# Kernel optimization log

Measured on AMD Instinct MI355X. Metric: run time of the kernel, lower is better.

Reference implementation:

```python
import jax, jax.numpy as jnp
import numpy as np

N_NODES = 50000
N_RAND_EDGES = 800000  # plus N_NODES self-loop edges appended in setup
IN_FEATS, N_HIDDEN, N_CLASSES = 128, 64, 64


def setup_inputs() -> dict:
    key = jax.random.key(0)
    kf, ks, kd, k1, k2, k3 = jax.random.split(key, 6)
    features = jax.random.normal(kf, (N_NODES, IN_FEATS), dtype=jnp.float32)
    src = jax.random.randint(ks, (N_RAND_EDGES,), 0, N_NODES, dtype=jnp.int32)
    dst = jax.random.randint(kd, (N_RAND_EDGES,), 0, N_NODES, dtype=jnp.int32)
    # dgl.add_self_loop: append (i, i) for every node
    loop = jnp.arange(N_NODES, dtype=jnp.int32)
    src = jnp.concatenate([src, loop])
    dst = jnp.concatenate([dst, loop])

    def glorot(k, fan_in, fan_out):
        lim = jnp.sqrt(6.0 / (fan_in + fan_out)).astype(jnp.float32)
        return jax.random.uniform(k, (fan_in, fan_out), jnp.float32, -lim, lim)

    return {
        "features": features, "src": src, "dst": dst,
        "W1": glorot(k1, IN_FEATS, N_HIDDEN), "b1": jnp.zeros((N_HIDDEN,), jnp.float32),
        "W2": glorot(k2, N_HIDDEN, N_HIDDEN), "b2": jnp.zeros((N_HIDDEN,), jnp.float32),
        "W3": glorot(k3, N_HIDDEN, N_CLASSES), "b3": jnp.zeros((N_CLASSES,), jnp.float32),
    }


def _graph_conv(x, W, b, src, dst, norm_src_e, norm_dst_n, n_nodes):
    """DGL GraphConv, norm='both': D_dst^{-1/2} A D_src^{-1/2} X W + b, then relu."""
    if W.shape[0] > W.shape[1]:  # mult by W first when it shrinks the feature dim
        x = x @ W
        m = x[src] * norm_src_e[:, None]                      # [E, out]
        h = jax.ops.segment_sum(m, dst, num_segments=n_nodes)  # [N, out]
        h = h * norm_dst_n[:, None]
    else:
        m = x[src] * norm_src_e[:, None]                      # [E, in]
        h = jax.ops.segment_sum(m, dst, num_segments=n_nodes)  # [N, in]
        h = (h * norm_dst_n[:, None]) @ W
    return jax.nn.relu(h + b)


def reference(features, src, dst, W1, b1, W2, b2, W3, b3):
    n = features.shape[0]
    ones = jnp.ones(src.shape[0], dtype=features.dtype)
    out_deg = jax.ops.segment_sum(ones, src, num_segments=n)
    in_deg = jax.ops.segment_sum(ones, dst, num_segments=n)
    norm_out = jnp.where(out_deg > 0, jax.lax.rsqrt(jnp.maximum(out_deg, 1.0)), 0.0)
    norm_in = jnp.where(in_deg > 0, jax.lax.rsqrt(jnp.maximum(in_deg, 1.0)), 0.0)
    norm_src_e = norm_out[src]  # per-edge source normalization

    h1 = _graph_conv(features, W1, b1, src, dst, norm_src_e, norm_in, n)
    h2 = _graph_conv(h1, W2, b2, src, dst, norm_src_e, norm_in, n)
    h3 = _graph_conv(h2, W3, b3, src, dst, norm_src_e, norm_in, n)
    # JumpingKnowledge mode='max': elementwise max over stacked layer outputs
    return jnp.max(jnp.stack([h1, h2, h3], axis=0), axis=0)
```

## Files before the change

### kernel.cpp

```cpp
#include <hip/hip_runtime.h>

typedef _Float16 h16;
typedef __attribute__((ext_vector_type(4))) _Float16 half4;

#define RANGES 8
#define PPR    32
#define HTHREADS 1024
#define BINS   6400
#define HALF   (BINS / 2)
#define HWORDS (BINS)

__global__ __launch_bounds__(HTHREADS) void hist_kernel(const int* __restrict__ src,
                                                        const int* __restrict__ dst,
                                                        int* __restrict__ partial, int E) {
  __shared__ int h[HWORDS];
  const int r = blockIdx.x >> 5;
  const int c = blockIdx.x & 31;
  for (int i = threadIdx.x; i < HWORDS; i += HTHREADS) h[i] = 0;
  __syncthreads();
  const int lo = r * BINS;
  const int chunk = (E + PPR - 1) / PPR;
  const int e0 = c * chunk;
  const int e1 = min(E, e0 + chunk);
  for (int e = e0 + threadIdx.x; e < e1; e += HTHREADS) {
    int s = src[e] - lo;
    if ((unsigned)s < (unsigned)BINS) atomicAdd(&h[s >> 1], 1 << ((s & 1) * 16));
    int d = dst[e] - lo;
    if ((unsigned)d < (unsigned)BINS) atomicAdd(&h[HALF + (d >> 1)], 1 << ((d & 1) * 16));
  }
  __syncthreads();
  int* op = partial + (size_t)blockIdx.x * HWORDS;
  for (int i = threadIdx.x; i < HWORDS; i += HTHREADS) op[i] = h[i];
}

__global__ __launch_bounds__(256) void reduce_norm_scan1(
    int* __restrict__ partial, float* __restrict__ nout, float* __restrict__ nin,
    int* __restrict__ rowptr, int* __restrict__ bsums, int N) {
  __shared__ int s[256];
  const int j = blockIdx.x * 256 + threadIdx.x;
  const int r = j / HALF;
  const int w = j % HALF;
  int* base = partial + (size_t)(r * PPR) * HWORDS;
  int sumO = 0, runI = 0;
#pragma unroll 8
  for (int p = 0; p < PPR; ++p) {
    sumO += base[(size_t)p * HWORDS + w];
    int vI = base[(size_t)p * HWORDS + HALF + w];
    base[(size_t)p * HWORDS + HALF + w] = runI;
    runI += vI;
  }
  const int od0 = sumO & 0xFFFF, od1 = (sumO >> 16) & 0xFFFF;
  const int id0 = runI & 0xFFFF, id1 = (runI >> 16) & 0xFFFF;
  const int n0 = 2 * j, n1 = 2 * j + 1;
  if (n0 < N) {
    nout[n0] = od0 > 0 ? rsqrtf((float)od0) : 0.f;
    nin[n0]  = id0 > 0 ? rsqrtf((float)id0) : 0.f;
  }
  if (n1 < N) {
    nout[n1] = od1 > 0 ? rsqrtf((float)od1) : 0.f;
    nin[n1]  = id1 > 0 ? rsqrtf((float)id1) : 0.f;
  }
  const int local = id0 + id1;
  int v = local;
  s[threadIdx.x] = v;
  __syncthreads();
#pragma unroll
  for (int off = 1; off < 256; off <<= 1) {
    int tv = 0;
    if (threadIdx.x >= off) tv = s[threadIdx.x - off];
    __syncthreads();
    if (threadIdx.x >= off) s[threadIdx.x] += tv;
    __syncthreads();
  }
  const int excl = s[threadIdx.x] - v;
  if (n0 < N) rowptr[n0] = excl;
  if (n1 < N) rowptr[n1] = excl + id0;
  if (threadIdx.x == 255) bsums[blockIdx.x] = s[255];
}

__global__ void scan_top(int* __restrict__ bsums, int nb) {
  __shared__ int s[256];
  __shared__ int run_s;
  if (threadIdx.x == 0) run_s = 0;
  __syncthreads();
  for (int base = 0; base < nb; base += 256) {
    int i = base + threadIdx.x;
    int v = (i < nb) ? bsums[i] : 0;
    s[threadIdx.x] = v;
    __syncthreads();
#pragma unroll
    for (int off = 1; off < 256; off <<= 1) {
      int tv = 0;
      if (threadIdx.x >= off) tv = s[threadIdx.x - off];
      __syncthreads();
      if (threadIdx.x >= off) s[threadIdx.x] += tv;
      __syncthreads();
    }
    int run = run_s;
    if (i < nb) bsums[i] = run + s[threadIdx.x] - v;
    __syncthreads();
    if (threadIdx.x == 0) run_s = run + s[255];
    __syncthreads();
  }
}

__global__ void add_off(int* __restrict__ rowptr, const int* __restrict__ bsums, int N, int E) {
  int i = blockIdx.x * 512 + threadIdx.x;
  if (i < N) rowptr[i] += bsums[blockIdx.x];
  if (blockIdx.x == 0 && threadIdx.x == 0) rowptr[N] = E;
}

__global__ __launch_bounds__(HTHREADS) void fill_kernel(
    const int* __restrict__ src, const int* __restrict__ dst,
    const int* __restrict__ rowptr, const int* __restrict__ partial,
    int* __restrict__ csr, int N, int E) {
  __shared__ int cur[BINS];
  const int r = blockIdx.x & 7;
  const int c = blockIdx.x >> 3;
  const int lo = r * BINS;
  const int* pf = partial + (size_t)(r * PPR + c) * HWORDS + HALF;
  for (int n = threadIdx.x; n < BINS; n += HTHREADS) {
    int g = lo + n;
    int rp = (g < N) ? rowptr[g] : 0;
    int pw = pf[n >> 1];
    cur[n] = rp + ((pw >> ((n & 1) * 16)) & 0xFFFF);
  }
  __syncthreads();
  const int chunk = (E + PPR - 1) / PPR;
  const int e0 = c * chunk;
  const int e1 = min(E, e0 + chunk);
  for (int e = e0 + threadIdx.x; e < e1; e += HTHREADS) {
    int d = dst[e] - lo;
    if ((unsigned)d < (unsigned)BINS) {
      int pos = atomicAdd(&cur[d], 1);
      csr[pos] = src[e];
    }
  }
}

template <bool L1>
__global__ void agg_kernel(const int* __restrict__ rowptr, const int* __restrict__ csr,
                           const h16* __restrict__ x, const float* __restrict__ nin,
                           const float* __restrict__ bias, const float* __restrict__ nout,
                           void* __restrict__ y, float* __restrict__ out, int N) {
  int t = blockIdx.x * blockDim.x + threadIdx.x;
  int node = t >> 4;
  if (node >= N) return;
  int lane = t & 15;
  const int b = rowptr[node], e = rowptr[node + 1];
  const half4* xv = reinterpret_cast<const half4*>(x);
  float4 a0 = make_float4(0.f, 0.f, 0.f, 0.f);
  float4 a1 = make_float4(0.f, 0.f, 0.f, 0.f);
  float4 a2 = make_float4(0.f, 0.f, 0.f, 0.f);
  float4 a3 = make_float4(0.f, 0.f, 0.f, 0.f);
  int i = b;
  for (; i + 4 <= e; i += 4) {
    int s0 = csr[i + 0], s1 = csr[i + 1], s2 = csr[i + 2], s3 = csr[i + 3];
    half4 v0 = xv[(size_t)s0 * 16 + lane];
    half4 v1 = xv[(size_t)s1 * 16 + lane];
    half4 v2 = xv[(size_t)s2 * 16 + lane];
    half4 v3 = xv[(size_t)s3 * 16 + lane];
    a0.x += (float)v0.x; a0.y += (float)v0.y; a0.z += (float)v0.z; a0.w += (float)v0.w;
    a1.x += (float)v1.x; a1.y += (float)v1.y; a1.z += (float)v1.z; a1.w += (float)v1.w;
    a2.x += (float)v2.x; a2.y += (float)v2.y; a2.z += (float)v2.z; a2.w += (float)v2.w;
    a3.x += (float)v3.x; a3.y += (float)v3.y; a3.z += (float)v3.z; a3.w += (float)v3.w;
  }
  for (; i < e; ++i) {
    int s = csr[i];
    half4 v = xv[(size_t)s * 16 + lane];
    a0.x += (float)v.x; a0.y += (float)v.y; a0.z += (float)v.z; a0.w += (float)v.w;
  }
  float4 acc;
  acc.x = (a0.x + a1.x) + (a2.x + a3.x);
  acc.y = (a0.y + a1.y) + (a2.y + a3.y);
  acc.z = (a0.z + a1.z) + (a2.z + a3.z);
  acc.w = (a0.w + a1.w) + (a2.w + a3.w);

  if (L1) {
    float s = nin[node];
    float4 bb = *reinterpret_cast<const float4*>(bias + lane * 4);
    float4 h;
    h.x = fmaxf(acc.x * s + bb.x, 0.f);
    h.y = fmaxf(acc.y * s + bb.y, 0.f);
    h.z = fmaxf(acc.z * s + bb.z, 0.f);
    h.w = fmaxf(acc.w * s + bb.w, 0.f);
    *reinterpret_cast<float4*>(out + (size_t)node * 64 + lane * 4) = h;
    float no = nout[node];
    half4 hv;
    hv.x = (h16)(h.x * no); hv.y = (h16)(h.y * no);
    hv.z = (h16)(h.z * no); hv.w = (h16)(h.w * no);
    reinterpret_cast<half4*>(y)[(size_t)node * 16 + lane] = hv;
  } else {
    *reinterpret_cast<float4*>((float*)y + (size_t)node * 64 + lane * 4) = acc;
  }
}

template <int K, bool INSCALE, bool FUSED, bool WRITEC>
__global__ __launch_bounds__(256) void gemm_kernel(
    const float* __restrict__ A, const float* __restrict__ B,
    const float* __restrict__ nin, const float* __restrict__ bias,
    const float* __restrict__ nout,
    half4* __restrict__ C, float* __restrict__ out, int M) {
  __shared__ float sA[64][K + 4];
  __shared__ float sB[K][64];
  const int t = threadIdx.x;
  const int row0 = blockIdx.x * 64;

  for (int i = t * 4; i < 64 * K; i += 256 * 4) {
    int r = i / K, c = i % K;
    int gr = row0 + r;
    float4 v = make_float4(0.f, 0.f, 0.f, 0.f);
    if (gr < M) {
      v = *reinterpret_cast<const float4*>(A + (size_t)gr * K + c);
      if (INSCALE) {
        float s = nin[gr];
        v.x *= s; v.y *= s; v.z *= s; v.w *= s;
      }
    }
    *reinterpret_cast<float4*>(&sA[r][c]) = v;
  }
  for (int i = t * 4; i < K * 64; i += 256 * 4) {
    *reinterpret_cast<float4*>(&sB[0][0] + i) = *reinterpret_cast<const float4*>(B + i);
  }
  __syncthreads();

  const int ty = t >> 4;
  const int tx = t & 15;
  float acc[4][4] = {};
#pragma unroll 8
  for (int k = 0; k < K; ++k) {
    float a[4];
#pragma unroll
    for (int i = 0; i < 4; ++i) a[i] = sA[ty * 4 + i][k];
    float4 b = *reinterpret_cast<float4*>(&sB[k][tx * 4]);
#pragma unroll
    for (int i = 0; i < 4; ++i) {
      acc[i][0] += a[i] * b.x;
      acc[i][1] += a[i] * b.y;
      acc[i][2] += a[i] * b.z;
      acc[i][3] += a[i] * b.w;
    }
  }

#pragma unroll
  for (int i = 0; i < 4; ++i) {
    int gr = row0 + ty * 4 + i;
    if (gr >= M) continue;
    float4 h = make_float4(acc[i][0], acc[i][1], acc[i][2], acc[i][3]);
    if (FUSED) {
      float4 b = *reinterpret_cast<const float4*>(bias + tx * 4);
      h.x = fmaxf(h.x + b.x, 0.f);
      h.y = fmaxf(h.y + b.y, 0.f);
      h.z = fmaxf(h.z + b.z, 0.f);
      h.w = fmaxf(h.w + b.w, 0.f);
      size_t off = (size_t)gr * 64 + tx * 4;
      float4 o = *reinterpret_cast<float4*>(out + off);
      o.x = fmaxf(o.x, h.x);
      o.y = fmaxf(o.y, h.y);
      o.z = fmaxf(o.z, h.z);
      o.w = fmaxf(o.w, h.w);
      *reinterpret_cast<float4*>(out + off) = o;
    }
    if (WRITEC) {
      float no = nout[gr];
      half4 hv;
      hv.x = (h16)(h.x * no); hv.y = (h16)(h.y * no);
      hv.z = (h16)(h.z * no); hv.w = (h16)(h.w * no);
      C[(size_t)gr * 16 + tx] = hv;
    }
  }
}

extern "C" void kernel_launch(void* const* d_in, const int* in_sizes, int n_in,
                              void* d_out, int out_size, void* d_ws, size_t ws_size,
                              hipStream_t stream) {
  const float* feat = (const float*)d_in[0];
  const int* src    = (const int*)d_in[1];
  const int* dst    = (const int*)d_in[2];
  const float* W1   = (const float*)d_in[3];
  const float* b1   = (const float*)d_in[4];
  const float* W2   = (const float*)d_in[5];
  const float* b2   = (const float*)d_in[6];
  const float* W3   = (const float*)d_in[7];
  const float* b3   = (const float*)d_in[8];
  float* out = (float*)d_out;

  const int N = in_sizes[0] / 128;
  const int E = in_sizes[1];

  char* p = (char*)d_ws;
  float* nout   = (float*)p;          p += (size_t)N * 4;
  float* nin    = (float*)p;          p += (size_t)N * 4;
  int*   rowptr = (int*)p;            p += ((size_t)N + 8) * 4;
  int*   bsums  = (int*)p;            p += 1024 * 4;
  int*   csr    = (int*)p;            p += (size_t)E * 4;
  p = (char*)(((uintptr_t)p + 15) & ~(uintptr_t)15);
  h16*   bufAh  = (h16*)p;            p += (size_t)N * 64 * 2;
  h16*   bufBh  = (h16*)p;            p += (size_t)N * 64 * 2;
  p = (char*)(((uintptr_t)p + 15) & ~(uintptr_t)15);
  float* bufF   = (float*)p;          p += (size_t)N * 64 * 4;
  int*   partial = (int*)bufF;

  const int nwords = RANGES * HALF;
  const int nb = nwords / 256;

  hist_kernel<<<RANGES * PPR, HTHREADS, 0, stream>>>(src, dst, partial, E);
  reduce_norm_scan1<<<nb, 256, 0, stream>>>(partial, nout, nin, rowptr, bsums, N);
  scan_top<<<1, 256, 0, stream>>>(bsums, nb);
  add_off<<<nb, 512, 0, stream>>>(rowptr, bsums, N, E);
  fill_kernel<<<RANGES * PPR, HTHREADS, 0, stream>>>(src, dst, rowptr, partial, csr, N, E);

  const int gemm_blocks = (N + 63) / 64;
  const int agg_blocks  = (N * 16 + 255) / 256;

  gemm_kernel<128, false, false, true><<<gemm_blocks, 256, 0, stream>>>(
      feat, W1, nullptr, nullptr, nout, (half4*)bufAh, nullptr, N);
  agg_kernel<true><<<agg_blocks, 256, 0, stream>>>(rowptr, csr, bufAh, nin, b1, nout, bufBh, out, N);

  agg_kernel<false><<<agg_blocks, 256, 0, stream>>>(rowptr, csr, bufBh, nullptr, nullptr, nullptr, bufF, nullptr, N);
  gemm_kernel<64, true, true, true><<<gemm_blocks, 256, 0, stream>>>(
      bufF, W2, nin, b2, nout, (half4*)bufAh, out, N);

  agg_kernel<false><<<agg_blocks, 256, 0, stream>>>(rowptr, csr, bufAh, nullptr, nullptr, nullptr, bufF, nullptr, N);
  gemm_kernel<64, true, true, false><<<gemm_blocks, 256, 0, stream>>>(
      bufF, W3, nin, b3, nullptr, nullptr, out, N);
}
```

Before: 171.8 us.

## Fuse aggregation into GEMM for layers 2-3, merge scan kernels, widen gathers

Layers 2 and 3 now compute the neighbor aggregation directly into shared memory and run the 64x64 GEMM in the same kernel, so the fp32 intermediate buffer is never written to or read back from global memory. The separate top-level scan kernel is folded into the offset-add kernel, and each block rescans the block sums itself. Gathers now use 8-wide half vectors with 8 lanes per node. The trade-off is that each fused block spends a long, uneven gather phase before the GEMM, with 512 threads and about 33KB of shared memory per block, which may reduce latency hiding.

```diff
diff --git a/kernel.cpp b/kernel.cpp
--- a/kernel.cpp
+++ b/kernel.cpp
@@ -2,6 +2,8 @@
 
 typedef _Float16 h16;
 typedef __attribute__((ext_vector_type(4))) _Float16 half4;
+typedef __attribute__((ext_vector_type(8))) _Float16 half8;
+typedef __attribute__((ext_vector_type(8))) float float8;
 
 #define RANGES 8
 #define PPR    32
@@ -78,36 +80,25 @@
   if (threadIdx.x == 255) bsums[blockIdx.x] = s[255];
 }
 
-__global__ void scan_top(int* __restrict__ bsums, int nb) {
-  __shared__ int s[256];
-  __shared__ int run_s;
-  if (threadIdx.x == 0) run_s = 0;
-  __syncthreads();
-  for (int base = 0; base < nb; base += 256) {
-    int i = base + threadIdx.x;
-    int v = (i < nb) ? bsums[i] : 0;
-    s[threadIdx.x] = v;
+__global__ __launch_bounds__(512) void add_off2(int* __restrict__ rowptr,
+                                                const int* __restrict__ bsums,
+                                                int N, int E, int nb) {
+  __shared__ int s[128];
+  const int tid = threadIdx.x;
+  if (tid < 128) s[tid] = (tid < nb) ? bsums[tid] : 0;
+  __syncthreads();
+#pragma unroll
+  for (int off = 1; off < 128; off <<= 1) {
+    int v = 0;
+    if (tid < 128 && tid >= off) v = s[tid - off];
     __syncthreads();
-#pragma unroll
-    for (int off = 1; off < 256; off <<= 1) {
-      int tv = 0;
-      if (threadIdx.x >= off) tv = s[threadIdx.x - off];
-      __syncthreads();
-      if (threadIdx.x >= off) s[threadIdx.x] += tv;
-      __syncthreads();
-    }
-    int run = run_s;
-    if (i < nb) bsums[i] = run + s[threadIdx.x] - v;
+    if (tid < 128 && tid >= off) s[tid] += v;
     __syncthreads();
-    if (threadIdx.x == 0) run_s = run + s[255];
-    __syncthreads();
-  }
-}
-
-__global__ void add_off(int* __restrict__ rowptr, const int* __restrict__ bsums, int N, int E) {
-  int i = blockIdx.x * 512 + threadIdx.x;
-  if (i < N) rowptr[i] += bsums[blockIdx.x];
-  if (blockIdx.x == 0 && threadIdx.x == 0) rowptr[N] = E;
+  }
+  const int base = (blockIdx.x == 0) ? 0 : s[blockIdx.x - 1];
+  const int i = blockIdx.x * 512 + tid;
+  if (i < N) rowptr[i] += base;
+  if (blockIdx.x == 0 && tid == 0) rowptr[N] = E;
 }
 
 __global__ __launch_bounds__(HTHREADS) void fill_kernel(
@@ -138,97 +129,158 @@
   }
 }
 
-template <bool L1>
-__global__ void agg_kernel(const int* __restrict__ rowptr, const int* __restrict__ csr,
-                           const h16* __restrict__ x, const float* __restrict__ nin,
-                           const float* __restrict__ bias, const float* __restrict__ nout,
-                           void* __restrict__ y, float* __restrict__ out, int N) {
-  int t = blockIdx.x * blockDim.x + threadIdx.x;
-  int node = t >> 4;
-  if (node >= N) return;
-  int lane = t & 15;
+__device__ __forceinline__ float8 gather_row(const int* __restrict__ rowptr,
+                                             const int* __restrict__ csr,
+                                             const half8* __restrict__ xv,
+                                             int node, int lane) {
   const int b = rowptr[node], e = rowptr[node + 1];
-  const half4* xv = reinterpret_cast<const half4*>(x);
-  float4 a0 = make_float4(0.f, 0.f, 0.f, 0.f);
-  float4 a1 = make_float4(0.f, 0.f, 0.f, 0.f);
-  float4 a2 = make_float4(0.f, 0.f, 0.f, 0.f);
-  float4 a3 = make_float4(0.f, 0.f, 0.f, 0.f);
+  float8 a0 = 0.f, a1 = 0.f, a2 = 0.f, a3 = 0.f;
   int i = b;
   for (; i + 4 <= e; i += 4) {
     int s0 = csr[i + 0], s1 = csr[i + 1], s2 = csr[i + 2], s3 = csr[i + 3];
-    half4 v0 = xv[(size_t)s0 * 16 + lane];
-    half4 v1 = xv[(size_t)s1 * 16 + lane];
-    half4 v2 = xv[(size_t)s2 * 16 + lane];
-    half4 v3 = xv[(size_t)s3 * 16 + lane];
-    a0.x += (float)v0.x; a0.y += (float)v0.y; a0.z += (float)v0.z; a0.w += (float)v0.w;
-    a1.x += (float)v1.x; a1.y += (float)v1.y; a1.z += (float)v1.z; a1.w += (float)v1.w;
-    a2.x += (float)v2.x; a2.y += (float)v2.y; a2.z += (float)v2.z; a2.w += (float)v2.w;
-    a3.x += (float)v3.x; a3.y += (float)v3.y; a3.z += (float)v3.z; a3.w += (float)v3.w;
+    half8 v0 = xv[(size_t)s0 * 8 + lane];
+    half8 v1 = xv[(size_t)s1 * 8 + lane];
+    half8 v2 = xv[(size_t)s2 * 8 + lane];
+    half8 v3 = xv[(size_t)s3 * 8 + lane];
+#pragma unroll
+    for (int j = 0; j < 8; ++j) {
+      a0[j] += (float)v0[j]; a1[j] += (float)v1[j];
+      a2[j] += (float)v2[j]; a3[j] += (float)v3[j];
+    }
   }
   for (; i < e; ++i) {
     int s = csr[i];
-    half4 v = xv[(size_t)s * 16 + lane];
-    a0.x += (float)v.x; a0.y += (float)v.y; a0.z += (float)v.z; a0.w += (float)v.w;
-  }
-  float4 acc;
-  acc.x = (a0.x + a1.x) + (a2.x + a3.x);
-  acc.y = (a0.y + a1.y) + (a2.y + a3.y);
-  acc.z = (a0.z + a1.z) + (a2.z + a3.z);
-  acc.w = (a0.w + a1.w) + (a2.w + a3.w);
-
-  if (L1) {
-    float s = nin[node];
-    float4 bb = *reinterpret_cast<const float4*>(bias + lane * 4);
-    float4 h;
-    h.x = fmaxf(acc.x * s + bb.x, 0.f);
-    h.y = fmaxf(acc.y * s + bb.y, 0.f);
-    h.z = fmaxf(acc.z * s + bb.z, 0.f);
-    h.w = fmaxf(acc.w * s + bb.w, 0.f);
-    *reinterpret_cast<float4*>(out + (size_t)node * 64 + lane * 4) = h;
-    float no = nout[node];
-    half4 hv;
-    hv.x = (h16)(h.x * no); hv.y = (h16)(h.y * no);
-    hv.z = (h16)(h.z * no); hv.w = (h16)(h.w * no);
-    reinterpret_cast<half4*>(y)[(size_t)node * 16 + lane] = hv;
-  } else {
-    *reinterpret_cast<float4*>((float*)y + (size_t)node * 64 + lane * 4) = acc;
-  }
-}
-
-template <int K, bool INSCALE, bool FUSED, bool WRITEC>
-__global__ __launch_bounds__(256) void gemm_kernel(
-    const float* __restrict__ A, const float* __restrict__ B,
+    half8 v = xv[(size_t)s * 8 + lane];
+#pragma unroll
+    for (int j = 0; j < 8; ++j) a0[j] += (float)v[j];
+  }
+#pragma unroll
+  for (int j = 0; j < 8; ++j) a0[j] = (a0[j] + a1[j]) + (a2[j] + a3[j]);
+  return a0;
+}
+
+__global__ __launch_bounds__(512) void agg1_kernel(
+    const int* __restrict__ rowptr, const int* __restrict__ csr,
+    const h16* __restrict__ x, const float* __restrict__ nin,
+    const float* __restrict__ bias, const float* __restrict__ nout,
+    half8* __restrict__ y, float* __restrict__ out, int N) {
+  int t = blockIdx.x * 512 + threadIdx.x;
+  int node = t >> 3;
+  if (node >= N) return;
+  int lane = t & 7;
+  float8 acc = gather_row(rowptr, csr, reinterpret_cast<const half8*>(x), node, lane);
+  const float s = nin[node];
+  const float no = nout[node];
+  float8 h;
+  half8 hv;
+#pragma unroll
+  for (int j = 0; j < 8; ++j) {
+    h[j] = fmaxf(acc[j] * s + bias[lane * 8 + j], 0.f);
+    hv[j] = (h16)(h[j] * no);
+  }
+  float4 o0 = make_float4(h[0], h[1], h[2], h[3]);
+  float4 o1 = make_float4(h[4], h[5], h[6], h[7]);
+  size_t off = (size_t)node * 64 + lane * 8;
+  *reinterpret_cast<float4*>(out + off)     = o0;
+  *reinterpret_cast<float4*>(out + off + 4) = o1;
+  y[(size_t)node * 8 + lane] = hv;
+}
+
+template <bool WRITEC>
+__global__ __launch_bounds__(512) void fused_layer(
+    const int* __restrict__ rowptr, const int* __restrict__ csr,
+    const h16* __restrict__ x, const float* __restrict__ W,
     const float* __restrict__ nin, const float* __restrict__ bias,
     const float* __restrict__ nout,
-    half4* __restrict__ C, float* __restrict__ out, int M) {
-  __shared__ float sA[64][K + 4];
-  __shared__ float sB[K][64];
+    half4* __restrict__ C, float* __restrict__ out, int N) {
+  __shared__ float sA[64][68];
+  __shared__ float sB[64][64];
   const int t = threadIdx.x;
   const int row0 = blockIdx.x * 64;
 
-  for (int i = t * 4; i < 64 * K; i += 256 * 4) {
-    int r = i / K, c = i % K;
+  for (int i = t * 4; i < 64 * 64; i += 512 * 4)
+    *reinterpret_cast<float4*>(&sB[0][0] + i) = *reinterpret_cast<const float4*>(W + i);
+
+  {
+    const int node = t >> 3, lane = t & 7;
+    const int g = row0 + node;
+    float8 acc = 0.f;
+    float s = 0.f;
+    if (g < N) {
+      acc = gather_row(rowptr, csr, reinterpret_cast<const half8*>(x), g, lane);
+      s = nin[g];
+    }
+    float4 w0 = make_float4(acc[0] * s, acc[1] * s, acc[2] * s, acc[3] * s);
+    float4 w1 = make_float4(acc[4] * s, acc[5] * s, acc[6] * s, acc[7] * s);
+    *reinterpret_cast<float4*>(&sA[node][lane * 8])     = w0;
+    *reinterpret_cast<float4*>(&sA[node][lane * 8 + 4]) = w1;
+  }
+  __syncthreads();
+
+  const int tx = t & 15;
+  const int ry = t >> 4;
+  const int r0 = 2 * ry, r1 = 2 * ry + 1;
+  float4 acc0 = make_float4(0.f, 0.f, 0.f, 0.f);
+  float4 acc1 = make_float4(0.f, 0.f, 0.f, 0.f);
+#pragma unroll 8
+  for (int k = 0; k < 64; ++k) {
+    float a0 = sA[r0][k], a1 = sA[r1][k];
+    float4 b = *reinterpret_cast<float4*>(&sB[k][tx * 4]);
+    acc0.x += a0 * b.x; acc0.y += a0 * b.y; acc0.z += a0 * b.z; acc0.w += a0 * b.w;
+    acc1.x += a1 * b.x; acc1.y += a1 * b.y; acc1.z += a1 * b.z; acc1.w += a1 * b.w;
+  }
+
+  const float4 bb = *reinterpret_cast<const float4*>(bias + tx * 4);
+#pragma unroll
+  for (int rr = 0; rr < 2; ++rr) {
+    const int gr = row0 + (rr ? r1 : r0);
+    if (gr >= N) continue;
+    float4 v = rr ? acc1 : acc0;
+    v.x = fmaxf(v.x + bb.x, 0.f);
+    v.y = fmaxf(v.y + bb.y, 0.f);
+    v.z = fmaxf(v.z + bb.z, 0.f);
+    v.w = fmaxf(v.w + bb.w, 0.f);
+    size_t off = (size_t)gr * 64 + tx * 4;
+    float4 o = *reinterpret_cast<float4*>(out + off);
+    o.x = fmaxf(o.x, v.x);
+    o.y = fmaxf(o.y, v.y);
+    o.z = fmaxf(o.z, v.z);
+    o.w = fmaxf(o.w, v.w);
+    *reinterpret_cast<float4*>(out + off) = o;
+    if (WRITEC) {
+      float no = nout[gr];
+      half4 hv;
+      hv.x = (h16)(v.x * no); hv.y = (h16)(v.y * no);
+      hv.z = (h16)(v.z * no); hv.w = (h16)(v.w * no);
+      C[(size_t)gr * 16 + tx] = hv;
+    }
+  }
+}
+
+__global__ __launch_bounds__(256) void gemm1_kernel(
+    const float* __restrict__ A, const float* __restrict__ B,
+    const float* __restrict__ nout, half4* __restrict__ C, int M) {
+  __shared__ float sA[64][132];
+  __shared__ float sB[128][64];
+  const int t = threadIdx.x;
+  const int row0 = blockIdx.x * 64;
+
+  for (int i = t * 4; i < 64 * 128; i += 256 * 4) {
+    int r = i / 128, c = i % 128;
     int gr = row0 + r;
     float4 v = make_float4(0.f, 0.f, 0.f, 0.f);
-    if (gr < M) {
-      v = *reinterpret_cast<const float4*>(A + (size_t)gr * K + c);
-      if (INSCALE) {
-        float s = nin[gr];
-        v.x *= s; v.y *= s; v.z *= s; v.w *= s;
-      }
-    }
+    if (gr < M) v = *reinterpret_cast<const float4*>(A + (size_t)gr * 128 + c);
     *reinterpret_cast<float4*>(&sA[r][c]) = v;
   }
-  for (int i = t * 4; i < K * 64; i += 256 * 4) {
+  for (int i = t * 4; i < 128 * 64; i += 256 * 4)
     *reinterpret_cast<float4*>(&sB[0][0] + i) = *reinterpret_cast<const float4*>(B + i);
-  }
   __syncthreads();
 
   const int ty = t >> 4;
   const int tx = t & 15;
   float acc[4][4] = {};
 #pragma unroll 8
-  for (int k = 0; k < K; ++k) {
+  for (int k = 0; k < 128; ++k) {
     float a[4];
 #pragma unroll
     for (int i = 0; i < 4; ++i) a[i] = sA[ty * 4 + i][k];
@@ -246,28 +298,11 @@
   for (int i = 0; i < 4; ++i) {
     int gr = row0 + ty * 4 + i;
     if (gr >= M) continue;
-    float4 h = make_float4(acc[i][0], acc[i][1], acc[i][2], acc[i][3]);
-    if (FUSED) {
-      float4 b = *reinterpret_cast<const float4*>(bias + tx * 4);
-      h.x = fmaxf(h.x + b.x, 0.f);
-      h.y = fmaxf(h.y + b.y, 0.f);
-      h.z = fmaxf(h.z + b.z, 0.f);
-      h.w = fmaxf(h.w + b.w, 0.f);
-      size_t off = (size_t)gr * 64 + tx * 4;
-      float4 o = *reinterpret_cast<float4*>(out + off);
-      o.x = fmaxf(o.x, h.x);
-      o.y = fmaxf(o.y, h.y);
-      o.z = fmaxf(o.z, h.z);
-      o.w = fmaxf(o.w, h.w);
-      *reinterpret_cast<float4*>(out + off) = o;
-    }
-    if (WRITEC) {
-      float no = nout[gr];
-      half4 hv;
-      hv.x = (h16)(h.x * no); hv.y = (h16)(h.y * no);
-      hv.z = (h16)(h.z * no); hv.w = (h16)(h.w * no);
-      C[(size_t)gr * 16 + tx] = hv;
-    }
+    float no = nout[gr];
+    half4 hv;
+    hv.x = (h16)(acc[i][0] * no); hv.y = (h16)(acc[i][1] * no);
+    hv.z = (h16)(acc[i][2] * no); hv.w = (h16)(acc[i][3] * no);
+    C[(size_t)gr * 16 + tx] = hv;
   }
 }
 
@@ -297,31 +332,26 @@
   p = (char*)(((uintptr_t)p + 15) & ~(uintptr_t)15);
   h16*   bufAh  = (h16*)p;            p += (size_t)N * 64 * 2;
   h16*   bufBh  = (h16*)p;            p += (size_t)N * 64 * 2;
-  p = (char*)(((uintptr_t)p + 15) & ~(uintptr_t)15);
-  float* bufF   = (float*)p;          p += (size_t)N * 64 * 4;
-  int*   partial = (int*)bufF;
+  int*   partial = (int*)bufAh;
 
   const int nwords = RANGES * HALF;
   const int nb = nwords / 256;
 
   hist_kernel<<<RANGES * PPR, HTHREADS, 0, stream>>>(src, dst, partial, E);
   reduce_norm_scan1<<<nb, 256, 0, stream>>>(partial, nout, nin, rowptr, bsums, N);
-  scan_top<<<1, 256, 0, stream>>>(bsums, nb);
-  add_off<<<nb, 512, 0, stream>>>(rowptr, bsums, N, E);
+  add_off2<<<nb, 512, 0, stream>>>(rowptr, bsums, N, E, nb);
   fill_kernel<<<RANGES * PPR, HTHREADS, 0, stream>>>(src, dst, rowptr, partial, csr, N, E);
 
-  const int gemm_blocks = (N + 63) / 64;
-  const int agg_blocks  = (N * 16 + 255) / 256;
-
-  gemm_kernel<128, false, false, true><<<gemm_blocks, 256, 0, stream>>>(
-      feat, W1, nullptr, nullptr, nout, (half4*)bufAh, nullptr, N);
-  agg_kernel<true><<<agg_blocks, 256, 0, stream>>>(rowptr, csr, bufAh, nin, b1, nout, bufBh, out, N);
-
-  agg_kernel<false><<<agg_blocks, 256, 0, stream>>>(rowptr, csr, bufBh, nullptr, nullptr, nullptr, bufF, nullptr, N);
-  gemm_kernel<64, true, true, true><<<gemm_blocks, 256, 0, stream>>>(
-      bufF, W2, nin, b2, nout, (half4*)bufAh, out, N);
-
-  agg_kernel<false><<<agg_blocks, 256, 0, stream>>>(rowptr, csr, bufAh, nullptr, nullptr, nullptr, bufF, nullptr, N);
-  gemm_kernel<64, true, true, false><<<gemm_blocks, 256, 0, stream>>>(
-      bufF, W3, nin, b3, nullptr, nullptr, out, N);
-}
+  const int gemm_blocks  = (N + 63) / 64;
+  const int agg1_blocks  = (int)(((size_t)N * 8 + 511) / 512);
+
+  gemm1_kernel<<<gemm_blocks, 256, 0, stream>>>(feat, W1, nout, (half4*)bufAh, N);
+  agg1_kernel<<<agg1_blocks, 512, 0, stream>>>(rowptr, csr, bufAh, nin, b1, nout,
+                                               (half8*)bufBh, out, N);
+
+  fused_layer<true><<<gemm_blocks, 512, 0, stream>>>(rowptr, csr, bufBh, W2, nin, b2, nout,
+                                                     (half4*)bufAh, out, N);
+
+  fused_layer<false><<<gemm_blocks, 512, 0, stream>>>(rowptr, csr, bufAh, W3, nin, b3, nullptr,
+                                                      nullptr, out, N);
+}
```

Measured after the change: 167.3 us. 2.6% less time.
